# Kernel optimization log

Measured on AMD Instinct MI355X. Metric: run time of the kernel, lower is better.

## Reference

```python
import jax, jax.numpy as jnp
import numpy as np

B, L, D = 8, 8192, 1024
M = L // 4  # target_ratio=4 -> exactly L/4 boundaries per batch row (enforced in setup_inputs)


@jax.custom_vjp
def ste(x):
    # Forward: ones_like(x). Backward: pass gradient straight through.
    return jnp.ones_like(x)

def _ste_fwd(x):
    return jnp.ones_like(x), None

def _ste_bwd(_, g):
    return (g,)

ste.defvjp(_ste_fwd, _ste_bwd)


def _ema_combine(c1, c2):
    # Linear recurrence h = a*h_prev + b as an associative op (matches the
    # Hillis-Steele doubling scan in the torch source exactly).
    a1, b1 = c1
    a2, b2 = c2
    return (a1 * a2, a2[..., None] * b1 + b2)


def setup_inputs() -> dict:
    key = jax.random.key(0)
    k1, k2, k3, k4, k5 = jax.random.split(key, 5)
    x = jax.random.normal(k1, (B, L, D), jnp.float32)
    residual = jax.random.normal(k2, (B, L, D), jnp.float32)
    prob = jax.random.uniform(k3, (B, L), jnp.float32)
    # exactly M=L//4 True positions per row (random locations) -> static M
    r = jax.random.uniform(k4, (B, L))
    sel = jnp.argsort(r, axis=1)[:, :M]
    token_mask = jnp.zeros((B, L), bool).at[jnp.arange(B)[:, None], sel].set(True)
    state = jax.random.normal(k5, (B, D), jnp.float32)
    return {"x": x, "residual": residual, "prob": prob,
            "token_mask": token_mask, "state": state}


def reference(x, residual, prob, token_mask, state):
    # ---- Tokenizer: compact selected positions to the front (stable order) ----
    counts = token_mask.sum(axis=1)                       # (B,)
    order = jnp.argsort(~token_mask, axis=1)[:, :M]       # stable: True positions first, in order
    chunked = jnp.take_along_axis(x, order[:, :, None], axis=1)      # (B, M, D)
    chunk_probs = jnp.take_along_axis(prob, order, axis=1)           # (B, M)
    valid = jnp.arange(M)[None, :] < counts[:, None]                  # (B, M)
    chunk_probs = chunk_probs * valid                     # padded slots -> 0 (new_zeros semantics)

    # ---- EMA scan over compacted chunks ----
    decay = jnp.clip(1.0 - chunk_probs, 0.0, 1.0)         # (B, M)
    b = (1.0 - decay)[..., None] * chunked                # (B, M, D)
    b = b.at[:, 0].add(decay[:, 0, None] * state)         # fold initial state into b[0]
    _, ema = jax.lax.associative_scan(_ema_combine, (decay, b), axis=1)
    ema = ema * valid[..., None]

    # ---- DeTokenizer: scatter-expand back to (B, L, D) ----
    chunk_idx = jnp.cumsum(token_mask.astype(jnp.int32), axis=1) - 1  # (B, L)
    valid_pos = chunk_idx >= 0
    ci = jnp.clip(chunk_idx, 0, M - 1)
    long_states = jnp.take_along_axis(ema, ci[:, :, None], axis=1)    # (B, L, D)
    long_states = long_states * valid_pos[..., None]

    coef = ste(jnp.maximum(1.0 - prob, prob))             # forward: ones; bwd: STE
    long_states = long_states * coef[..., None]

    output = residual + long_states                       # (B, L, D)

    # new_state = last valid EMA value per batch (or carried-over state if empty)
    last = jnp.clip(counts - 1, 0, M - 1)
    new_state = jnp.take_along_axis(ema, last[:, None, None], axis=1)[:, 0]
    new_state = jnp.where((counts > 0)[:, None], new_state, state)
    return output, new_state
```

## Files before the change

kernel.cpp:

```cpp
#include <hip/hip_runtime.h>
#include <stdint.h>
#include <stddef.h>

#define B_ 8
#define L_ 8192
#define D_ 1024
#define M_ 2048
#define S_ 128
#define G_ 16
#define D4_ (D_/4)

typedef float f4 __attribute__((ext_vector_type(4)));

#define OFF_POS    ((size_t)0)
#define OFF_DEC    (OFF_POS  + (size_t)B_*M_*4)
#define OFF_A      (OFF_DEC  + (size_t)B_*M_*4)
#define OFF_EZ     (OFF_A    + (size_t)B_*S_*4)
#define OFF_HINIT  (OFF_EZ   + (size_t)B_*S_*D_*4)
#define WS_TOTAL   (OFF_HINIT + (size_t)B_*S_*D_*4)

__global__ __launch_bounds__(1024)
void compact_kernel(const void* __restrict__ mask_raw,
                    const float* __restrict__ prob,
                    int* __restrict__ pos,
                    float* __restrict__ dec) {
    const int b = blockIdx.x;
    const int t = threadIdx.x;

    __shared__ int u8flag;
    if (t == 0) u8flag = 0;
    __syncthreads();
    {
        const uint32_t* mu = (const uint32_t*)mask_raw;
        uint32_t w0 = mu[t * 2], w1 = mu[t * 2 + 1];
        if (w0 > 1u || w1 > 1u) atomicOr(&u8flag, 1);
    }
    __syncthreads();
    const bool u8 = (u8flag != 0);

    int mv[8];
    const int base_l = t * 8;
    if (u8) {
        const uint8_t* mrow = (const uint8_t*)mask_raw + (size_t)b * L_;
        #pragma unroll
        for (int j = 0; j < 8; j++) mv[j] = mrow[base_l + j] ? 1 : 0;
    } else {
        const int* mrow = (const int*)mask_raw + (size_t)b * L_;
        #pragma unroll
        for (int j = 0; j < 8; j++) mv[j] = mrow[base_l + j] ? 1 : 0;
    }
    int tsum = 0;
    #pragma unroll
    for (int j = 0; j < 8; j++) tsum += mv[j];

    const int lane = t & 63, wid = t >> 6;
    int v = tsum;
    #pragma unroll
    for (int off = 1; off < 64; off <<= 1) {
        int n = __shfl_up(v, off, 64);
        if (lane >= off) v += n;
    }
    __shared__ int wsum[16];
    __shared__ int woff[16];
    if (lane == 63) wsum[wid] = v;
    __syncthreads();
    if (t < 16) {
        int acc = 0;
        for (int w = 0; w < t; w++) acc += wsum[w];
        woff[t] = acc;
    }
    __syncthreads();
    int run = (v - tsum) + woff[wid];

    const float* prow = prob + (size_t)b * L_;
    #pragma unroll
    for (int j = 0; j < 8; j++) {
        const int l = base_l + j;
        if (mv[j]) {
            float d = 1.0f - prow[l];
            d = fminf(fmaxf(d, 0.0f), 1.0f);
            pos[(size_t)b * M_ + run] = l;
            dec[(size_t)b * M_ + run] = d;
            run += 1;
        }
    }
}

__global__ __launch_bounds__(256)
void segend_kernel(const f4* __restrict__ x4,
                   const int* __restrict__ pos,
                   const float* __restrict__ dec,
                   f4* __restrict__ ez4,
                   float* __restrict__ Aseg) {
    const int blk = blockIdx.x;
    const int b = blk / S_, s = blk % S_;
    const int t = threadIdx.x;
    __shared__ int   pl[G_];
    __shared__ float dl[G_];
    if (t < G_) {
        pl[t] = pos[(size_t)b * M_ + (size_t)s * G_ + t];
        dl[t] = dec[(size_t)b * M_ + (size_t)s * G_ + t];
    }
    __syncthreads();
    f4 h = (f4)(0.0f);
    #pragma unroll
    for (int m = 0; m < G_; m++) {
        const float d = dl[m];
        const f4 xv = x4[((size_t)b * L_ + pl[m]) * D4_ + t];
        h = d * h + (1.0f - d) * xv;
    }
    ez4[(size_t)blk * D4_ + t] = h;
    if (t == 0) {
        float p = 1.0f;
        #pragma unroll
        for (int m = 0; m < G_; m++) p *= dl[m];
        Aseg[blk] = p;
    }
}

__global__ __launch_bounds__(64)
void combine_kernel(const float* __restrict__ ez,
                    const float* __restrict__ Aseg,
                    const float* __restrict__ state,
                    float* __restrict__ hinit,
                    float* __restrict__ newstate) {
    const int b = blockIdx.x;
    const int ch = blockIdx.y * 64 + threadIdx.x;
    __shared__ float Al[S_];
    for (int i = threadIdx.x; i < S_; i += 64) Al[i] = Aseg[b * S_ + i];
    __syncthreads();

    float c = state[(size_t)b * D_ + ch];
    for (int s0 = 0; s0 < S_; s0 += 8) {
        float e[8];
        #pragma unroll
        for (int j = 0; j < 8; j++)
            e[j] = ez[((size_t)b * S_ + s0 + j) * D_ + ch];
        #pragma unroll
        for (int j = 0; j < 8; j++) {
            hinit[((size_t)b * S_ + s0 + j) * D_ + ch] = c;
            c = fmaf(Al[s0 + j], c, e[j]);
        }
    }
    newstate[(size_t)b * D_ + ch] = c;
}

__global__ __launch_bounds__(256)
void fused_kernel(const f4* __restrict__ x4,
                  const f4* __restrict__ res4,
                  const int* __restrict__ pos,
                  const float* __restrict__ dec,
                  const f4* __restrict__ hinit4,
                  f4* __restrict__ out4) {
    const int blk = blockIdx.x;
    const int b = blk / S_, s = blk % S_;
    const int t = threadIdx.x;
    __shared__ int   pl[G_ + 1];
    __shared__ float dl[G_];
    if (t < G_) {
        pl[t] = pos[(size_t)b * M_ + (size_t)s * G_ + t];
        dl[t] = dec[(size_t)b * M_ + (size_t)s * G_ + t];
    }
    if (t == 0) {
        pl[G_] = (s == S_ - 1) ? L_ : pos[(size_t)b * M_ + (size_t)(s + 1) * G_];
    }
    __syncthreads();

    const f4* xrow   = x4   + (size_t)b * L_ * D4_;
    const f4* resrow = res4 + (size_t)b * L_ * D4_;
    f4*       outrow = out4 + (size_t)b * L_ * D4_;

    if (s == 0) {
        const int p0 = pl[0];
        for (int l0 = 0; l0 < p0; l0++) {
            f4 r = __builtin_nontemporal_load(resrow + (size_t)l0 * D4_ + t);
            __builtin_nontemporal_store(r, outrow + (size_t)l0 * D4_ + t);
        }
    }

    f4 h = hinit4[(size_t)blk * D4_ + t];
    int m = -1;
    int nextb = pl[0];
    f4 xn  = xrow[(size_t)pl[0] * D4_ + t];
    f4 xn2 = xrow[(size_t)pl[1] * D4_ + t];
    int l = pl[0];
    const int lend = pl[G_];

    #define ADV(K, HH)                                                    \
        if (l + (K) == nextb) {                                           \
            ++m;                                                          \
            const float d_ = dl[m];                                       \
            h = d_ * h + (1.0f - d_) * xn;                                \
            xn = xn2;                                                     \
            nextb = pl[m + 1];                                            \
            const int ni_ = (m + 2 <= G_ - 1) ? pl[m + 2] : pl[0];        \
            xn2 = xrow[(size_t)ni_ * D4_ + t];                            \
        }                                                                 \
        HH = h;

    f4 c0, c1, c2, c3;
    if (l + 4 <= lend) {
        c0 = __builtin_nontemporal_load(resrow + (size_t)(l + 0) * D4_ + t);
        c1 = __builtin_nontemporal_load(resrow + (size_t)(l + 1) * D4_ + t);
        c2 = __builtin_nontemporal_load(resrow + (size_t)(l + 2) * D4_ + t);
        c3 = __builtin_nontemporal_load(resrow + (size_t)(l + 3) * D4_ + t);
    }
    while (l + 8 <= lend) {
        f4 n0 = __builtin_nontemporal_load(resrow + (size_t)(l + 4) * D4_ + t);
        f4 n1 = __builtin_nontemporal_load(resrow + (size_t)(l + 5) * D4_ + t);
        f4 n2 = __builtin_nontemporal_load(resrow + (size_t)(l + 6) * D4_ + t);
        f4 n3 = __builtin_nontemporal_load(resrow + (size_t)(l + 7) * D4_ + t);
        f4 h0, h1, h2, h3;
        ADV(0, h0); ADV(1, h1); ADV(2, h2); ADV(3, h3);
        __builtin_nontemporal_store(c0 + h0, outrow + (size_t)(l + 0) * D4_ + t);
        __builtin_nontemporal_store(c1 + h1, outrow + (size_t)(l + 1) * D4_ + t);
        __builtin_nontemporal_store(c2 + h2, outrow + (size_t)(l + 2) * D4_ + t);
        __builtin_nontemporal_store(c3 + h3, outrow + (size_t)(l + 3) * D4_ + t);
        c0 = n0; c1 = n1; c2 = n2; c3 = n3;
        l += 4;
    }
    if (l + 4 <= lend) {
        f4 h0, h1, h2, h3;
        ADV(0, h0); ADV(1, h1); ADV(2, h2); ADV(3, h3);
        __builtin_nontemporal_store(c0 + h0, outrow + (size_t)(l + 0) * D4_ + t);
        __builtin_nontemporal_store(c1 + h1, outrow + (size_t)(l + 1) * D4_ + t);
        __builtin_nontemporal_store(c2 + h2, outrow + (size_t)(l + 2) * D4_ + t);
        __builtin_nontemporal_store(c3 + h3, outrow + (size_t)(l + 3) * D4_ + t);
        l += 4;
    }
    for (; l < lend; l++) {
        f4 hh;
        ADV(0, hh);
        f4 r = __builtin_nontemporal_load(resrow + (size_t)l * D4_ + t);
        __builtin_nontemporal_store(r + hh, outrow + (size_t)l * D4_ + t);
    }
    #undef ADV
}

extern "C" void kernel_launch(void* const* d_in, const int* in_sizes, int n_in,
                              void* d_out, int out_size, void* d_ws, size_t ws_size,
                              hipStream_t stream) {
    const float* x        = (const float*)d_in[0];
    const float* residual = (const float*)d_in[1];
    const float* prob     = (const float*)d_in[2];
    const void*  mask     = d_in[3];
    const float* state    = (const float*)d_in[4];

    float* out       = (float*)d_out;
    float* new_state = out + (size_t)B_ * L_ * D_;

    if (ws_size < WS_TOTAL) return;

    char* ws = (char*)d_ws;
    int*   pos   = (int*)  (ws + OFF_POS);
    float* dec   = (float*)(ws + OFF_DEC);
    float* Aseg  = (float*)(ws + OFF_A);
    float* ez    = (float*)(ws + OFF_EZ);
    float* hinit = (float*)(ws + OFF_HINIT);

    compact_kernel<<<B_, 1024, 0, stream>>>(mask, prob, pos, dec);

    segend_kernel<<<B_ * S_, 256, 0, stream>>>(
        (const f4*)x, pos, dec, (f4*)ez, Aseg);

    combine_kernel<<<dim3(B_, 16), 64, 0, stream>>>(
        ez, Aseg, state, hinit, new_state);

    fused_kernel<<<B_ * S_, 256, 0, stream>>>(
        (const f4*)x, (const f4*)residual, pos, dec,
        (const f4*)hinit, (f4*)out);
}
```

Measured before the change: 146.8 us.

## Split expand kernel into fixed 64-row output tiles instead of segment-bounded work

The final expand kernel now assigns each block a fixed tile of 64 output rows rather than the variable span between 16-boundary segments. The compaction kernel records the chunk index at each tile start. Each block reconstructs its starting EMA state by replaying up to 16 steps from the segment's hinit, and uses a live flag for rows before the first boundary. This balances per-block work, since segment spans vary randomly and the first block also had to copy the leading prefix, at the cost of redundant gathers of x for the replay.

```diff
diff --git a/kernel.cpp b/kernel.cpp
--- a/kernel.cpp
+++ b/kernel.cpp
@@ -9,13 +9,16 @@
 #define S_ 128
 #define G_ 16
 #define D4_ (D_/4)
+#define TROWS_ 64
+#define NTILE_ (L_/TROWS_)
 
 typedef float f4 __attribute__((ext_vector_type(4)));
 
 #define OFF_POS    ((size_t)0)
 #define OFF_DEC    (OFF_POS  + (size_t)B_*M_*4)
 #define OFF_A      (OFF_DEC  + (size_t)B_*M_*4)
-#define OFF_EZ     (OFF_A    + (size_t)B_*S_*4)
+#define OFF_CIT    (OFF_A    + (size_t)B_*S_*4)
+#define OFF_EZ     (OFF_CIT  + (size_t)B_*NTILE_*4)
 #define OFF_HINIT  (OFF_EZ   + (size_t)B_*S_*D_*4)
 #define WS_TOTAL   (OFF_HINIT + (size_t)B_*S_*D_*4)
 
@@ -23,7 +26,8 @@
 void compact_kernel(const void* __restrict__ mask_raw,
                     const float* __restrict__ prob,
                     int* __restrict__ pos,
-                    float* __restrict__ dec) {
+                    float* __restrict__ dec,
+                    int* __restrict__ ci_tile) {
     const int b = blockIdx.x;
     const int t = threadIdx.x;
 
@@ -83,6 +87,10 @@
             dec[(size_t)b * M_ + run] = d;
             run += 1;
         }
+    }
+    if ((t & 7) == 7) {
+        const int k = (t + 1) >> 3;
+        if (k < NTILE_) ci_tile[b * NTILE_ + k] = run - 1;
     }
 }
 
@@ -106,8 +114,7 @@
     #pragma unroll
     for (int m = 0; m < G_; m++) {
         const float d = dl[m];
-        const f4 xv = x4[((size_t)b * L_ + pl[m]) * D4_ + t];
-        h = d * h + (1.0f - d) * xv;
+        h = d * h + (1.0f - d) * x4[((size_t)b * L_ + pl[m]) * D4_ + t];
     }
     ez4[(size_t)blk * D4_ + t] = h;
     if (t == 0) {
@@ -150,89 +157,106 @@
                   const f4* __restrict__ res4,
                   const int* __restrict__ pos,
                   const float* __restrict__ dec,
+                  const int* __restrict__ ci_tile,
+                  const float* __restrict__ state,
                   const f4* __restrict__ hinit4,
                   f4* __restrict__ out4) {
     const int blk = blockIdx.x;
-    const int b = blk / S_, s = blk % S_;
+    const int b = blk >> 7;
+    const int k = blk & (NTILE_ - 1);
     const int t = threadIdx.x;
-    __shared__ int   pl[G_ + 1];
-    __shared__ float dl[G_];
-    if (t < G_) {
-        pl[t] = pos[(size_t)b * M_ + (size_t)s * G_ + t];
-        dl[t] = dec[(size_t)b * M_ + (size_t)s * G_ + t];
-    }
-    if (t == 0) {
-        pl[G_] = (s == S_ - 1) ? L_ : pos[(size_t)b * M_ + (size_t)(s + 1) * G_];
-    }
-    __syncthreads();
-
-    const f4* xrow   = x4   + (size_t)b * L_ * D4_;
+    const int l0 = k * TROWS_;
+
+    const int m0 = (k == 0) ? -1 : ci_tile[b * NTILE_ + k];
+
+    __shared__ int   pl[TROWS_ + 2];
+    __shared__ float dl[TROWS_ + 2];
+    if (t < TROWS_ + 2) {
+        const int mm = m0 + 1 + t;
+        if (mm < M_) {
+            pl[t] = pos[(size_t)b * M_ + mm];
+            dl[t] = dec[(size_t)b * M_ + mm];
+        } else {
+            pl[t] = L_;
+            dl[t] = 1.0f;
+        }
+    }
+    __syncthreads();
+
+    const f4* xrow = x4 + (size_t)b * L_ * D4_;
+
+    f4 h;
+    float live;
+    if (m0 < 0) {
+        h = ((const f4*)state)[(size_t)b * D4_ + t];
+        live = 0.0f;
+    } else {
+        const int s0 = m0 >> 4;
+        const int mbase = s0 << 4;
+        h = hinit4[((size_t)b * S_ + s0) * D4_ + t];
+        live = 1.0f;
+        #pragma unroll
+        for (int j = 0; j < G_; j++) {
+            const int mj = mbase + j;
+            const float draw = dec[(size_t)b * M_ + mj];
+            const float d = (mj <= m0) ? draw : 1.0f;
+            const f4 xv = xrow[(size_t)pos[(size_t)b * M_ + mj] * D4_ + t];
+            h = d * h + (1.0f - d) * xv;
+        }
+    }
+
     const f4* resrow = res4 + (size_t)b * L_ * D4_;
     f4*       outrow = out4 + (size_t)b * L_ * D4_;
 
-    if (s == 0) {
-        const int p0 = pl[0];
-        for (int l0 = 0; l0 < p0; l0++) {
-            f4 r = __builtin_nontemporal_load(resrow + (size_t)l0 * D4_ + t);
-            __builtin_nontemporal_store(r, outrow + (size_t)l0 * D4_ + t);
-        }
-    }
-
-    f4 h = hinit4[(size_t)blk * D4_ + t];
-    int m = -1;
+    int mi = 0;
     int nextb = pl[0];
-    f4 xn  = xrow[(size_t)pl[0] * D4_ + t];
-    f4 xn2 = xrow[(size_t)pl[1] * D4_ + t];
-    int l = pl[0];
-    const int lend = pl[G_];
-
-    #define ADV(K, HH)                                                    \
+    int a0 = (pl[0] < L_) ? pl[0] : 0;
+    int a1 = (pl[1] < L_) ? pl[1] : 0;
+    f4 xn  = xrow[(size_t)a0 * D4_ + t];
+    f4 xn2 = xrow[(size_t)a1 * D4_ + t];
+    int l = l0;
+
+    #define ADV(K, HH, LV)                                                \
         if (l + (K) == nextb) {                                           \
-            ++m;                                                          \
-            const float d_ = dl[m];                                       \
+            const float d_ = dl[mi];                                      \
             h = d_ * h + (1.0f - d_) * xn;                                \
+            live = 1.0f;                                                  \
             xn = xn2;                                                     \
-            nextb = pl[m + 1];                                            \
-            const int ni_ = (m + 2 <= G_ - 1) ? pl[m + 2] : pl[0];        \
-            xn2 = xrow[(size_t)ni_ * D4_ + t];                            \
+            ++mi;                                                         \
+            nextb = pl[mi];                                               \
+            const int nr_ = (pl[mi + 1] < L_) ? pl[mi + 1] : 0;           \
+            xn2 = xrow[(size_t)nr_ * D4_ + t];                            \
         }                                                                 \
-        HH = h;
+        HH = h; LV = live;
 
     f4 c0, c1, c2, c3;
-    if (l + 4 <= lend) {
-        c0 = __builtin_nontemporal_load(resrow + (size_t)(l + 0) * D4_ + t);
-        c1 = __builtin_nontemporal_load(resrow + (size_t)(l + 1) * D4_ + t);
-        c2 = __builtin_nontemporal_load(resrow + (size_t)(l + 2) * D4_ + t);
-        c3 = __builtin_nontemporal_load(resrow + (size_t)(l + 3) * D4_ + t);
-    }
-    while (l + 8 <= lend) {
+    c0 = __builtin_nontemporal_load(resrow + (size_t)(l + 0) * D4_ + t);
+    c1 = __builtin_nontemporal_load(resrow + (size_t)(l + 1) * D4_ + t);
+    c2 = __builtin_nontemporal_load(resrow + (size_t)(l + 2) * D4_ + t);
+    c3 = __builtin_nontemporal_load(resrow + (size_t)(l + 3) * D4_ + t);
+    for (int g = 0; g < (TROWS_ / 4) - 1; ++g) {
         f4 n0 = __builtin_nontemporal_load(resrow + (size_t)(l + 4) * D4_ + t);
         f4 n1 = __builtin_nontemporal_load(resrow + (size_t)(l + 5) * D4_ + t);
         f4 n2 = __builtin_nontemporal_load(resrow + (size_t)(l + 6) * D4_ + t);
         f4 n3 = __builtin_nontemporal_load(resrow + (size_t)(l + 7) * D4_ + t);
         f4 h0, h1, h2, h3;
-        ADV(0, h0); ADV(1, h1); ADV(2, h2); ADV(3, h3);
-        __builtin_nontemporal_store(c0 + h0, outrow + (size_t)(l + 0) * D4_ + t);
-        __builtin_nontemporal_store(c1 + h1, outrow + (size_t)(l + 1) * D4_ + t);
-        __builtin_nontemporal_store(c2 + h2, outrow + (size_t)(l + 2) * D4_ + t);
-        __builtin_nontemporal_store(c3 + h3, outrow + (size_t)(l + 3) * D4_ + t);
+        float v0, v1, v2, v3;
+        ADV(0, h0, v0); ADV(1, h1, v1); ADV(2, h2, v2); ADV(3, h3, v3);
+        __builtin_nontemporal_store(c0 + v0 * h0, outrow + (size_t)(l + 0) * D4_ + t);
+        __builtin_nontemporal_store(c1 + v1 * h1, outrow + (size_t)(l + 1) * D4_ + t);
+        __builtin_nontemporal_store(c2 + v2 * h2, outrow + (size_t)(l + 2) * D4_ + t);
+        __builtin_nontemporal_store(c3 + v3 * h3, outrow + (size_t)(l + 3) * D4_ + t);
         c0 = n0; c1 = n1; c2 = n2; c3 = n3;
         l += 4;
     }
-    if (l + 4 <= lend) {
+    {
         f4 h0, h1, h2, h3;
-        ADV(0, h0); ADV(1, h1); ADV(2, h2); ADV(3, h3);
-        __builtin_nontemporal_store(c0 + h0, outrow + (size_t)(l + 0) * D4_ + t);
-        __builtin_nontemporal_store(c1 + h1, outrow + (size_t)(l + 1) * D4_ + t);
-        __builtin_nontemporal_store(c2 + h2, outrow + (size_t)(l + 2) * D4_ + t);
-        __builtin_nontemporal_store(c3 + h3, outrow + (size_t)(l + 3) * D4_ + t);
-        l += 4;
-    }
-    for (; l < lend; l++) {
-        f4 hh;
-        ADV(0, hh);
-        f4 r = __builtin_nontemporal_load(resrow + (size_t)l * D4_ + t);
-        __builtin_nontemporal_store(r + hh, outrow + (size_t)l * D4_ + t);
+        float v0, v1, v2, v3;
+        ADV(0, h0, v0); ADV(1, h1, v1); ADV(2, h2, v2); ADV(3, h3, v3);
+        __builtin_nontemporal_store(c0 + v0 * h0, outrow + (size_t)(l + 0) * D4_ + t);
+        __builtin_nontemporal_store(c1 + v1 * h1, outrow + (size_t)(l + 1) * D4_ + t);
+        __builtin_nontemporal_store(c2 + v2 * h2, outrow + (size_t)(l + 2) * D4_ + t);
+        __builtin_nontemporal_store(c3 + v3 * h3, outrow + (size_t)(l + 3) * D4_ + t);
     }
     #undef ADV
 }
@@ -252,13 +276,14 @@
     if (ws_size < WS_TOTAL) return;
 
     char* ws = (char*)d_ws;
-    int*   pos   = (int*)  (ws + OFF_POS);
-    float* dec   = (float*)(ws + OFF_DEC);
-    float* Aseg  = (float*)(ws + OFF_A);
-    float* ez    = (float*)(ws + OFF_EZ);
-    float* hinit = (float*)(ws + OFF_HINIT);
-
-    compact_kernel<<<B_, 1024, 0, stream>>>(mask, prob, pos, dec);
+    int*   pos     = (int*)  (ws + OFF_POS);
+    float* dec     = (float*)(ws + OFF_DEC);
+    float* Aseg    = (float*)(ws + OFF_A);
+    int*   ci_tile = (int*)  (ws + OFF_CIT);
+    float* ez      = (float*)(ws + OFF_EZ);
+    float* hinit   = (float*)(ws + OFF_HINIT);
+
+    compact_kernel<<<B_, 1024, 0, stream>>>(mask, prob, pos, dec, ci_tile);
 
     segend_kernel<<<B_ * S_, 256, 0, stream>>>(
         (const f4*)x, pos, dec, (f4*)ez, Aseg);
@@ -266,7 +291,7 @@
     combine_kernel<<<dim3(B_, 16), 64, 0, stream>>>(
         ez, Aseg, state, hinit, new_state);
 
-    fused_kernel<<<B_ * S_, 256, 0, stream>>>(
-        (const f4*)x, (const f4*)residual, pos, dec,
+    fused_kernel<<<B_ * NTILE_, 256, 0, stream>>>(
+        (const f4*)x, (const f4*)residual, pos, dec, ci_tile, state,
         (const f4*)hinit, (f4*)out);
 }
```

New measurement: 140.0 us. 1.05x faster.
